# Performance work log

Measured on AMD Instinct MI355X. Metric: run time of the kernel, lower is better.

The kernel has to match this reference:

```python
import jax, jax.numpy as jnp
import numpy as np

# ---- model dims (match init_kwargs) ----
IN_DIM, HID, OUT, BRANCH = 700, 512, 20, 4
VTH = 1.0
B, T = 256, 250


def _make_mask(rng):
    # DH-SNN dendritic mask: for each hidden neuron, a random permutation of the
    # (padded) inputs is split into BRANCH contiguous groups; branch j of neuron i
    # only sees its group.  pad = ((IN//BR)*BR + BR - IN) % BR == 0 for 700/4.
    mask = np.zeros((HID * BRANCH, IN_DIM), dtype=np.float32)
    per = IN_DIM // BRANCH
    for i in range(HID):
        seq = rng.permutation(IN_DIM)
        for j in range(BRANCH):
            mask[i * BRANCH + j, seq[j * per:(j + 1) * per]] = 1.0
    return jnp.asarray(mask)


def setup_inputs() -> dict:
    key = jax.random.key(0)
    ks = jax.random.split(key, 8)
    x = jax.random.normal(ks[0], (B, T, IN_DIM), dtype=jnp.float32)
    # nn.Linear(IN, HID*BRANCH) style init
    lim1 = 1.0 / np.sqrt(IN_DIM)
    w1 = jax.random.uniform(ks[1], (HID * BRANCH, IN_DIM), jnp.float32, -lim1, lim1)
    b1 = jax.random.uniform(ks[2], (HID * BRANCH,), jnp.float32, -lim1, lim1)
    # tau initializer 'uniform' in [low_m, high_m] = [0, 4]
    tau_m1 = jax.random.uniform(ks[3], (HID,), jnp.float32, 0.0, 4.0)
    tau_n1 = jax.random.uniform(ks[4], (HID, BRANCH), jnp.float32, 0.0, 4.0)
    lim2 = 1.0 / np.sqrt(HID)
    w2 = jax.random.uniform(ks[5], (OUT, HID), jnp.float32, -lim2, lim2)
    b2 = jax.random.uniform(ks[6], (OUT,), jnp.float32, -lim2, lim2)
    tau_m2 = jax.random.uniform(ks[7], (OUT,), jnp.float32, 0.0, 4.0)
    mask = _make_mask(np.random.default_rng(0))
    return {"x": x, "w1": w1, "b1": b1, "tau_m1": tau_m1, "tau_n1": tau_n1,
            "mask": mask, "w2": w2, "b2": b2, "tau_m2": tau_m2}


# surrogate-gradient spike (ActFun_adp with gaussian surrogate; fwd = heaviside)
GAMMA, LENS = 0.5, 0.5

@jax.custom_vjp
def spike_fn(v):
    return (v > 0).astype(v.dtype)

def _spike_fwd(v):
    return spike_fn(v), v

def _spike_bwd(v, g):
    sg = GAMMA * jnp.exp(-(v * v) / (2.0 * LENS * LENS)) / jnp.sqrt(2.0 * jnp.pi * LENS * LENS)
    return (g * sg,)

spike_fn.defvjp(_spike_fwd, _spike_bwd)


def reference(x, w1, b1, tau_m1, tau_n1, mask, w2, b2, tau_m2):
    Bb, Tt, _ = x.shape
    H, K = tau_n1.shape
    O = tau_m2.shape[0]
    eff_w = w1 * mask                                   # masked dendritic weights
    # precompute branch currents for all timesteps in one GEMM: (B,T,H*K)
    cur = jnp.einsum('bti,hi->bth', x, eff_w) + b1
    cur = cur.reshape(Bb, Tt, H, K)
    beta = jax.nn.sigmoid(tau_n1)                        # (H,K) dendritic decay
    alpha = jax.nn.sigmoid(tau_m1)                       # (H,)  soma decay
    alpha2 = jax.nn.sigmoid(tau_m2)                      # (O,)  readout decay

    def step(carry, c_t):
        d, mem1, spk, mem2 = carry
        d = beta * d + (1.0 - beta) * c_t                # dendritic membrane
        l = d.sum(-1)                                    # (B,H) summed branches (wotanh)
        mem1 = alpha * mem1 + (1.0 - alpha) * l - VTH * spk  # soft reset
        spk = spike_fn(mem1 - VTH)
        mem2 = alpha2 * mem2 + (1.0 - alpha2) * (spk @ w2.T + b2)  # leaky readout
        return (d, mem1, spk, mem2), mem2

    init = (jnp.zeros((Bb, H, K), x.dtype), jnp.zeros((Bb, H), x.dtype),
            jnp.zeros((Bb, H), x.dtype), jnp.zeros((Bb, O), x.dtype))
    _, outs = jax.lax.scan(step, init, jnp.swapaxes(cur, 0, 1))
    return jnp.swapaxes(outs, 0, 1)                      # (B,T,O)
```

## Files before the change

kernel.cpp:

```cpp
#include <hip/hip_runtime.h>
#include <hip/hip_bf16.h>
#include <hip/hip_fp16.h>

#define BATCH 256
#define TSTEPS 250
#define INDIM 700
#define KPAD 704
#define HID 512
#define HK 2048
#define NOUT 20
#define NCHUNK 66

typedef __attribute__((ext_vector_type(8))) _Float16 f16x8;
typedef __attribute__((ext_vector_type(4))) _Float16 f16x4;
typedef __attribute__((ext_vector_type(4))) float f32x4;

__device__ __forceinline__ float sigf(float x) { return 1.0f / (1.0f + expf(-x)); }

__device__ __forceinline__ void gload_lds16(const void* g, void* l) {
    __builtin_amdgcn_global_load_lds(
        (const __attribute__((address_space(1))) void*)g,
        (__attribute__((address_space(3))) void*)l, 16, 0, 0);
}

__global__ __launch_bounds__(192) void split_x(
    const float* __restrict__ x, _Float16* __restrict__ X0,
    _Float16* __restrict__ X1, int t0, int tc) {
    const int row = blockIdx.x;
    const int b = row / tc, tt = row - b * tc;
    const float* xr = x + (size_t)(b * TSTEPS + t0 + tt) * INDIM;
    const int k = threadIdx.x * 4;
    if (k >= KPAD) return;
    float4 v = {0.f, 0.f, 0.f, 0.f};
    if (k < INDIM) v = *(const float4*)(xr + k);
    f16x4 h, l;
    h[0] = (_Float16)v.x; l[0] = (_Float16)(v.x - (float)h[0]);
    h[1] = (_Float16)v.y; l[1] = (_Float16)(v.y - (float)h[1]);
    h[2] = (_Float16)v.z; l[2] = (_Float16)(v.z - (float)h[2]);
    h[3] = (_Float16)v.w; l[3] = (_Float16)(v.w - (float)h[3]);
    *(f16x4*)(X0 + (size_t)row * KPAD + k) = h;
    *(f16x4*)(X1 + (size_t)row * KPAD + k) = l;
}

__global__ __launch_bounds__(192) void split_w(
    const float* __restrict__ w1, const float* __restrict__ mask,
    _Float16* __restrict__ W0, _Float16* __restrict__ W1) {
    const int n = blockIdx.x;
    const int k = threadIdx.x * 4;
    if (k >= KPAD) return;
    float4 e = {0.f, 0.f, 0.f, 0.f};
    if (k < INDIM) {
        float4 wv = *(const float4*)(w1 + (size_t)n * INDIM + k);
        float4 mv = *(const float4*)(mask + (size_t)n * INDIM + k);
        e.x = wv.x * mv.x; e.y = wv.y * mv.y;
        e.z = wv.z * mv.z; e.w = wv.w * mv.w;
    }
    f16x4 h, l;
    h[0] = (_Float16)e.x; l[0] = (_Float16)(e.x - (float)h[0]);
    h[1] = (_Float16)e.y; l[1] = (_Float16)(e.y - (float)h[1]);
    h[2] = (_Float16)e.z; l[2] = (_Float16)(e.z - (float)h[2]);
    h[3] = (_Float16)e.w; l[3] = (_Float16)(e.w - (float)h[3]);
    *(f16x4*)(W0 + (size_t)n * KPAD + k) = h;
    *(f16x4*)(W1 + (size_t)n * KPAD + k) = l;
}

__global__ __launch_bounds__(512, 1) void gemm_f16(
    const _Float16* __restrict__ X0, const _Float16* __restrict__ X1,
    const _Float16* __restrict__ W0, const _Float16* __restrict__ W1,
    const float* __restrict__ b1, float* __restrict__ C) {
    extern __shared__ char smem[];
    const int tid = threadIdx.x;
    const int w = tid >> 6, lane = tid & 63;
    const int wm = w >> 2, wn = w & 3;
    const int lm = lane & 15, cfr = lane >> 4;

    const int nwg = gridDim.x;
    const int cpx = nwg >> 3;
    const int o = blockIdx.x;
    const int wg = (o & 7) * cpx + (o >> 3);
    const int n0 = (wg & 7) * 256;
    const int m0 = (wg >> 3) * 256;

    size_t grA[2], grB[2];
#pragma unroll
    for (int i = 0; i < 2; ++i) {
        int pr = i * 64 + (tid >> 3);
        int p = tid & 7;
        int l = p ^ (pr & 7);
        int rr = 2 * pr + (l >> 2);
        int c = l & 3;
        grA[i] = (size_t)(m0 + rr) * (KPAD * 2) + (size_t)c * 16;
        grB[i] = (size_t)(n0 + rr) * (KPAD * 2) + (size_t)c * 16;
    }

    int aoff[8], boff[4];
#pragma unroll
    for (int mf = 0; mf < 8; ++mf) {
        int row = wm * 128 + mf * 16 + lm;
        int pr = row >> 1, l = (row & 1) * 4 + cfr, p = l ^ (pr & 7);
        aoff[mf] = pr * 128 + p * 16;
    }
#pragma unroll
    for (int nf = 0; nf < 4; ++nf) {
        int row = wn * 64 + nf * 16 + lm;
        int pr = row >> 1, l = (row & 1) * 4 + cfr, p = l ^ (pr & 7);
        boff[nf] = pr * 128 + p * 16;
    }

    auto stageA = [&](int js) {
        int seg = (js >= 44) ? 2 : (js >= 22 ? 1 : 0);
        const char* base = (const char*)((seg < 2) ? X0 : X1);
        size_t ko = (size_t)(js - seg * 22) * 64;
        char* l0 = smem + (js & 3) * 32768 + w * 1024;
        gload_lds16(base + grA[0] + ko, l0);
        gload_lds16(base + grA[1] + ko, l0 + 8192);
    };
    auto stageB = [&](int js) {
        int seg = (js >= 44) ? 2 : (js >= 22 ? 1 : 0);
        const char* base = (const char*)((seg == 1) ? W1 : W0);
        size_t ko = (size_t)(js - seg * 22) * 64;
        char* l0 = smem + (js & 3) * 32768 + 16384 + w * 1024;
        gload_lds16(base + grB[0] + ko, l0);
        gload_lds16(base + grB[1] + ko, l0 + 8192);
    };

    f32x4 acc[8][4];
#pragma unroll
    for (int mf = 0; mf < 8; ++mf)
#pragma unroll
        for (int nf = 0; nf < 4; ++nf) acc[mf][nf] = (f32x4){0.f, 0.f, 0.f, 0.f};

    stageA(0); stageB(0); stageA(1); stageB(1);
    asm volatile("s_waitcnt vmcnt(4)" ::: "memory");
    __builtin_amdgcn_s_barrier();
    __builtin_amdgcn_sched_barrier(0);

    for (int j = 0; j < NCHUNK; ++j) {
        const char* sa = smem + (j & 3) * 32768;
        const char* sb = sa + 16384;
        f16x8 alo[4], bf[4];
#pragma unroll
        for (int mf = 0; mf < 4; ++mf)
            alo[mf] = *(const f16x8*)(sa + aoff[mf]);
#pragma unroll
        for (int nf = 0; nf < 4; ++nf)
            bf[nf] = *(const f16x8*)(sb + boff[nf]);
        if (j + 2 < NCHUNK) stageA(j + 2);
        __builtin_amdgcn_s_barrier();
        __builtin_amdgcn_sched_barrier(0);
        __builtin_amdgcn_s_setprio(1);
#pragma unroll
        for (int mf = 0; mf < 4; ++mf)
#pragma unroll
            for (int nf = 0; nf < 4; ++nf)
                acc[mf][nf] = __builtin_amdgcn_mfma_f32_16x16x32_f16(
                    alo[mf], bf[nf], acc[mf][nf], 0, 0, 0);
        __builtin_amdgcn_s_setprio(0);
        __builtin_amdgcn_s_barrier();
        __builtin_amdgcn_sched_barrier(0);
        f16x8 ahi[4];
#pragma unroll
        for (int mf = 0; mf < 4; ++mf)
            ahi[mf] = *(const f16x8*)(sa + aoff[4 + mf]);
        if (j + 2 < NCHUNK) stageB(j + 2);
        if (j < NCHUNK - 2)
            asm volatile("s_waitcnt vmcnt(4)" ::: "memory");
        else
            asm volatile("s_waitcnt vmcnt(0)" ::: "memory");
        __builtin_amdgcn_s_barrier();
        __builtin_amdgcn_sched_barrier(0);
        __builtin_amdgcn_s_setprio(1);
#pragma unroll
        for (int mf = 0; mf < 4; ++mf)
#pragma unroll
            for (int nf = 0; nf < 4; ++nf)
                acc[4 + mf][nf] = __builtin_amdgcn_mfma_f32_16x16x32_f16(
                    ahi[mf], bf[nf], acc[4 + mf][nf], 0, 0, 0);
        __builtin_amdgcn_s_setprio(0);
        __builtin_amdgcn_s_barrier();
        __builtin_amdgcn_sched_barrier(0);
    }

    const int crow0 = m0 + wm * 128 + (lane >> 4) * 4;
    const int ccol0 = n0 + wn * 64 + lm;
#pragma unroll
    for (int nf = 0; nf < 4; ++nf) {
        const float bias = b1[ccol0 + nf * 16];
#pragma unroll
        for (int mf = 0; mf < 8; ++mf) {
            f32x4 v = acc[mf][nf];
            const int r0 = crow0 + mf * 16;
#pragma unroll
            for (int r = 0; r < 4; ++r)
                C[(size_t)(r0 + r) * HK + ccol0 + nf * 16] = v[r] + bias;
        }
    }
}

__global__ __launch_bounds__(256) void snn_scan(
    const float* __restrict__ Cur,
    const float* __restrict__ tau_m1,
    const float* __restrict__ tau_n1,
    float* __restrict__ st_d,
    float* __restrict__ st_m1,
    unsigned long long* __restrict__ spk,
    int t0, int tc) {
    const int b = blockIdx.x;
    const int tid = threadIdx.x;
    const int h0 = tid, h1 = tid + 256;
    const int wid = tid >> 6, lane = tid & 63;

    const float a0 = sigf(tau_m1[h0]);
    const float a1 = sigf(tau_m1[h1]);
    const float oma0 = 1.0f - a0, oma1 = 1.0f - a1;
    float4 tb0 = *(const float4*)(tau_n1 + h0 * 4);
    float4 tb1 = *(const float4*)(tau_n1 + h1 * 4);
    float be0[4] = {sigf(tb0.x), sigf(tb0.y), sigf(tb0.z), sigf(tb0.w)};
    float be1[4] = {sigf(tb1.x), sigf(tb1.y), sigf(tb1.z), sigf(tb1.w)};
    float ob0[4] = {1.0f - be0[0], 1.0f - be0[1], 1.0f - be0[2], 1.0f - be0[3]};
    float ob1[4] = {1.0f - be1[0], 1.0f - be1[1], 1.0f - be1[2], 1.0f - be1[3]};

    float d0[4], d1[4], m10, m11, s0, s1;
    if (t0 == 0) {
#pragma unroll
        for (int k = 0; k < 4; ++k) { d0[k] = 0.0f; d1[k] = 0.0f; }
        m10 = 0.0f; m11 = 0.0f; s0 = 0.0f; s1 = 0.0f;
    } else {
        float4 dv0 = *(const float4*)(st_d + (size_t)b * HK + tid * 4);
        float4 dv1 = *(const float4*)(st_d + (size_t)b * HK + 1024 + tid * 4);
        d0[0] = dv0.x; d0[1] = dv0.y; d0[2] = dv0.z; d0[3] = dv0.w;
        d1[0] = dv1.x; d1[1] = dv1.y; d1[2] = dv1.z; d1[3] = dv1.w;
        m10 = st_m1[(size_t)b * HID + h0];
        m11 = st_m1[(size_t)b * HID + h1];
        const unsigned long long* sp = spk + ((size_t)b * TSTEPS + (t0 - 1)) * 8;
        s0 = ((sp[wid] >> lane) & 1ull) ? 1.0f : 0.0f;
        s1 = ((sp[4 + wid] >> lane) & 1ull) ? 1.0f : 0.0f;
    }

    const float* cbase = Cur + (size_t)b * tc * HK;
    float4 c0 = *(const float4*)(cbase + tid * 4);
    float4 c1 = *(const float4*)(cbase + 1024 + tid * 4);

    for (int tt = 0; tt < tc; ++tt) {
        float4 n0v, n1v;
        if (tt + 1 < tc) {
            const float* p = cbase + (size_t)(tt + 1) * HK;
            n0v = *(const float4*)(p + tid * 4);
            n1v = *(const float4*)(p + 1024 + tid * 4);
        } else { n0v = c0; n1v = c1; }

        d0[0] = be0[0] * d0[0] + ob0[0] * c0.x;
        d0[1] = be0[1] * d0[1] + ob0[1] * c0.y;
        d0[2] = be0[2] * d0[2] + ob0[2] * c0.z;
        d0[3] = be0[3] * d0[3] + ob0[3] * c0.w;
        d1[0] = be1[0] * d1[0] + ob1[0] * c1.x;
        d1[1] = be1[1] * d1[1] + ob1[1] * c1.y;
        d1[2] = be1[2] * d1[2] + ob1[2] * c1.z;
        d1[3] = be1[3] * d1[3] + ob1[3] * c1.w;
        float l0 = (d0[0] + d0[1]) + (d0[2] + d0[3]);
        float l1 = (d1[0] + d1[1]) + (d1[2] + d1[3]);

        m10 = a0 * m10 + oma0 * l0 - s0;
        m11 = a1 * m11 + oma1 * l1 - s1;
        bool sp0 = m10 > 1.0f;
        bool sp1 = m11 > 1.0f;
        s0 = sp0 ? 1.0f : 0.0f;
        s1 = sp1 ? 1.0f : 0.0f;

        unsigned long long mk0 = __ballot(sp0);
        unsigned long long mk1 = __ballot(sp1);
        if (lane == 0) {
            unsigned long long* ox = spk + ((size_t)b * TSTEPS + (t0 + tt)) * 8;
            ox[wid] = mk0;
            ox[4 + wid] = mk1;
        }
        c0 = n0v; c1 = n1v;
    }

    float4 dv0 = {d0[0], d0[1], d0[2], d0[3]};
    float4 dv1 = {d1[0], d1[1], d1[2], d1[3]};
    *(float4*)(st_d + (size_t)b * HK + tid * 4) = dv0;
    *(float4*)(st_d + (size_t)b * HK + 1024 + tid * 4) = dv1;
    st_m1[(size_t)b * HID + h0] = m10;
    st_m1[(size_t)b * HID + h1] = m11;
}

__global__ __launch_bounds__(256) void spk_gemm(
    const unsigned long long* __restrict__ spk,
    const float* __restrict__ w2,
    const float* __restrict__ b2,
    float* __restrict__ Y) {
    __shared__ float w2t[512][21];
    const int t = blockIdx.x;
    const int b = threadIdx.x;
    for (int i = threadIdx.x; i < HID * NOUT; i += 256) {
        int o = i / HID;
        int h = i - o * HID;
        w2t[h][o] = w2[i];
    }
    __syncthreads();
    float acc[NOUT];
#pragma unroll
    for (int o = 0; o < NOUT; ++o) acc[o] = b2[o];
    const unsigned long long* sp = spk + ((size_t)b * TSTEPS + t) * 8;
#pragma unroll
    for (int w = 0; w < 8; ++w) {
        unsigned long long m = sp[w];
        while (m) {
            int i = __ffsll((long long)m) - 1;
            m &= m - 1;
            const float* col = &w2t[w * 64 + i][0];
#pragma unroll
            for (int o = 0; o < NOUT; ++o) acc[o] += col[o];
        }
    }
    float* outp = Y + ((size_t)b * TSTEPS + t) * NOUT;
#pragma unroll
    for (int o = 0; o < NOUT; ++o) outp[o] = acc[o];
}

__global__ __launch_bounds__(256) void filter_out(
    float* __restrict__ Y, const float* __restrict__ tau_m2) {
    int gid = blockIdx.x * 256 + threadIdx.x;
    if (gid >= BATCH * NOUT) return;
    int b = gid / NOUT;
    int o = gid - b * NOUT;
    float a2 = sigf(tau_m2[o]);
    float oma = 1.0f - a2;
    float m2 = 0.0f;
    float* p = Y + (size_t)b * TSTEPS * NOUT + o;
    for (int t = 0; t < TSTEPS; ++t) {
        m2 = a2 * m2 + oma * p[(size_t)t * NOUT];
        p[(size_t)t * NOUT] = m2;
    }
}

extern "C" void kernel_launch(void* const* d_in, const int* in_sizes, int n_in,
                              void* d_out, int out_size, void* d_ws, size_t ws_size,
                              hipStream_t stream) {
    const float* x      = (const float*)d_in[0];
    const float* w1     = (const float*)d_in[1];
    const float* b1     = (const float*)d_in[2];
    const float* tau_m1 = (const float*)d_in[3];
    const float* tau_n1 = (const float*)d_in[4];
    const float* mask   = (const float*)d_in[5];
    const float* w2     = (const float*)d_in[6];
    const float* b2     = (const float*)d_in[7];
    const float* tau_m2 = (const float*)d_in[8];
    float* out = (float*)d_out;

    char* ws = (char*)d_ws;
    size_t off = 0;
    auto walloc = [&](size_t bytes) -> void* {
        void* p = ws + off;
        off += (bytes + 255) & ~(size_t)255;
        return p;
    };
    _Float16* W0 = (_Float16*)walloc((size_t)HK * KPAD * 2);
    _Float16* W1 = (_Float16*)walloc((size_t)HK * KPAD * 2);
    unsigned long long* spk =
        (unsigned long long*)walloc((size_t)BATCH * TSTEPS * 8 * 8);
    float* st_d  = (float*)walloc((size_t)BATCH * HK * 4);
    float* st_m1 = (float*)walloc((size_t)BATCH * HID * 4);

    const size_t perT = (size_t)BATCH * HK * 4 + 2 * (size_t)BATCH * KPAD * 2;
    size_t avail = (ws_size > off + 4096) ? ws_size - off - 4096 : 0;
    int Tc = (int)(avail / perT);
    if (Tc > TSTEPS) Tc = TSTEPS;
    if (Tc < 1) Tc = 1;
    _Float16* X0 = (_Float16*)walloc((size_t)BATCH * Tc * KPAD * 2);
    _Float16* X1 = (_Float16*)walloc((size_t)BATCH * Tc * KPAD * 2);
    float* cur   = (float*)walloc((size_t)BATCH * Tc * HK * 4);

    split_w<<<HK, 192, 0, stream>>>(w1, mask, W0, W1);

    for (int t0 = 0; t0 < TSTEPS; t0 += Tc) {
        int tc = (TSTEPS - t0 < Tc) ? (TSTEPS - t0) : Tc;
        split_x<<<BATCH * tc, 192, 0, stream>>>(x, X0, X1, t0, tc);
        dim3 grid(8 * tc);
        gemm_f16<<<grid, 512, 131072, stream>>>(X0, X1, W0, W1, b1, cur);
        snn_scan<<<BATCH, 256, 0, stream>>>(cur, tau_m1, tau_n1, st_d, st_m1,
                                            spk, t0, tc);
    }
    spk_gemm<<<TSTEPS, 256, 0, stream>>>(spk, w2, b2, out);
    filter_out<<<(BATCH * NOUT + 255) / 256, 256, 0, stream>>>(out, tau_m2);
}
```

Before: 1.133 ms.

## Use 32x32 MFMA with deeper prefetch, split scan blocks, chunk readout filter

The GEMM moves from 16x16x32 to 32x32x16 MFMA tiles. It also stages three chunks ahead instead of two and drops half the barriers per iteration. The SNN scan now launches two blocks per batch row, each with one neuron per thread, to double parallelism. The serial readout leaky filter becomes a three-pass chunked scan (partial, combine, fix-up with powf decay) so more threads work on it. These changes raise MFMA efficiency and latency hiding, at the cost of more accumulator registers, extra kernel launches, and slight rounding differences in the filter.

After: 1.148 ms. About the same (+1.3%).

```diff
diff --git a/kernel.cpp b/kernel.cpp
--- a/kernel.cpp
+++ b/kernel.cpp
@@ -10,10 +10,13 @@
 #define HK 2048
 #define NOUT 20
 #define NCHUNK 66
+#define FCH 10
+#define FCL 25
 
 typedef __attribute__((ext_vector_type(8))) _Float16 f16x8;
 typedef __attribute__((ext_vector_type(4))) _Float16 f16x4;
 typedef __attribute__((ext_vector_type(4))) float f32x4;
+typedef __attribute__((ext_vector_type(16))) float f32x16;
 
 __device__ __forceinline__ float sigf(float x) { return 1.0f / (1.0f + expf(-x)); }
 
@@ -72,7 +75,7 @@
     const int tid = threadIdx.x;
     const int w = tid >> 6, lane = tid & 63;
     const int wm = w >> 2, wn = w & 3;
-    const int lm = lane & 15, cfr = lane >> 4;
+    const int lr = lane & 31, cl = lane >> 5;
 
     const int nwg = gridDim.x;
     const int cpx = nwg >> 3;
@@ -93,19 +96,25 @@
         grB[i] = (size_t)(n0 + rr) * (KPAD * 2) + (size_t)c * 16;
     }
 
-    int aoff[8], boff[4];
-#pragma unroll
-    for (int mf = 0; mf < 8; ++mf) {
-        int row = wm * 128 + mf * 16 + lm;
-        int pr = row >> 1, l = (row & 1) * 4 + cfr, p = l ^ (pr & 7);
-        aoff[mf] = pr * 128 + p * 16;
-    }
-#pragma unroll
-    for (int nf = 0; nf < 4; ++nf) {
-        int row = wn * 64 + nf * 16 + lm;
-        int pr = row >> 1, l = (row & 1) * 4 + cfr, p = l ^ (pr & 7);
-        boff[nf] = pr * 128 + p * 16;
-    }
+    int aoff[4][2], boff[2][2];
+#pragma unroll
+    for (int mb = 0; mb < 4; ++mb)
+#pragma unroll
+        for (int ks = 0; ks < 2; ++ks) {
+            int row = wm * 128 + mb * 32 + lr;
+            int c = ks * 2 + cl;
+            int pr = row >> 1, l = (row & 1) * 4 + c, p = l ^ (pr & 7);
+            aoff[mb][ks] = pr * 128 + p * 16;
+        }
+#pragma unroll
+    for (int nb = 0; nb < 2; ++nb)
+#pragma unroll
+        for (int ks = 0; ks < 2; ++ks) {
+            int row = wn * 64 + nb * 32 + lr;
+            int c = ks * 2 + cl;
+            int pr = row >> 1, l = (row & 1) * 4 + c, p = l ^ (pr & 7);
+            boff[nb][ks] = pr * 128 + p * 16;
+        }
 
     auto stageA = [&](int js) {
         int seg = (js >= 44) ? 2 : (js >= 22 ? 1 : 0);
@@ -124,75 +133,68 @@
         gload_lds16(base + grB[1] + ko, l0 + 8192);
     };
 
-    f32x4 acc[8][4];
-#pragma unroll
-    for (int mf = 0; mf < 8; ++mf)
-#pragma unroll
-        for (int nf = 0; nf < 4; ++nf) acc[mf][nf] = (f32x4){0.f, 0.f, 0.f, 0.f};
-
-    stageA(0); stageB(0); stageA(1); stageB(1);
-    asm volatile("s_waitcnt vmcnt(4)" ::: "memory");
+    f32x16 acc[4][2];
+#pragma unroll
+    for (int mb = 0; mb < 4; ++mb)
+#pragma unroll
+        for (int nb = 0; nb < 2; ++nb)
+#pragma unroll
+            for (int r = 0; r < 16; ++r) acc[mb][nb][r] = 0.f;
+
+    stageA(0); stageB(0); stageA(1); stageB(1); stageA(2); stageB(2);
+    asm volatile("s_waitcnt vmcnt(8)" ::: "memory");
     __builtin_amdgcn_s_barrier();
     __builtin_amdgcn_sched_barrier(0);
 
     for (int j = 0; j < NCHUNK; ++j) {
         const char* sa = smem + (j & 3) * 32768;
         const char* sb = sa + 16384;
-        f16x8 alo[4], bf[4];
-#pragma unroll
-        for (int mf = 0; mf < 4; ++mf)
-            alo[mf] = *(const f16x8*)(sa + aoff[mf]);
-#pragma unroll
-        for (int nf = 0; nf < 4; ++nf)
-            bf[nf] = *(const f16x8*)(sb + boff[nf]);
-        if (j + 2 < NCHUNK) stageA(j + 2);
-        __builtin_amdgcn_s_barrier();
-        __builtin_amdgcn_sched_barrier(0);
+        if (j + 3 < NCHUNK) { stageA(j + 3); stageB(j + 3); }
+        f16x8 af[4][2], bf[2][2];
+#pragma unroll
+        for (int mb = 0; mb < 4; ++mb)
+#pragma unroll
+            for (int ks = 0; ks < 2; ++ks)
+                af[mb][ks] = *(const f16x8*)(sa + aoff[mb][ks]);
+#pragma unroll
+        for (int nb = 0; nb < 2; ++nb)
+#pragma unroll
+            for (int ks = 0; ks < 2; ++ks)
+                bf[nb][ks] = *(const f16x8*)(sb + boff[nb][ks]);
         __builtin_amdgcn_s_setprio(1);
 #pragma unroll
-        for (int mf = 0; mf < 4; ++mf)
-#pragma unroll
-            for (int nf = 0; nf < 4; ++nf)
-                acc[mf][nf] = __builtin_amdgcn_mfma_f32_16x16x32_f16(
-                    alo[mf], bf[nf], acc[mf][nf], 0, 0, 0);
+        for (int ks = 0; ks < 2; ++ks)
+#pragma unroll
+            for (int mb = 0; mb < 4; ++mb)
+#pragma unroll
+                for (int nb = 0; nb < 2; ++nb)
+                    acc[mb][nb] = __builtin_amdgcn_mfma_f32_32x32x16_f16(
+                        af[mb][ks], bf[nb][ks], acc[mb][nb], 0, 0, 0);
         __builtin_amdgcn_s_setprio(0);
-        __builtin_amdgcn_s_barrier();
-        __builtin_amdgcn_sched_barrier(0);
-        f16x8 ahi[4];
-#pragma unroll
-        for (int mf = 0; mf < 4; ++mf)
-            ahi[mf] = *(const f16x8*)(sa + aoff[4 + mf]);
-        if (j + 2 < NCHUNK) stageB(j + 2);
-        if (j < NCHUNK - 2)
+        if (j < NCHUNK - 3)
+            asm volatile("s_waitcnt vmcnt(8)" ::: "memory");
+        else if (j == NCHUNK - 3)
             asm volatile("s_waitcnt vmcnt(4)" ::: "memory");
         else
             asm volatile("s_waitcnt vmcnt(0)" ::: "memory");
         __builtin_amdgcn_s_barrier();
         __builtin_amdgcn_sched_barrier(0);
-        __builtin_amdgcn_s_setprio(1);
-#pragma unroll
-        for (int mf = 0; mf < 4; ++mf)
-#pragma unroll
-            for (int nf = 0; nf < 4; ++nf)
-                acc[4 + mf][nf] = __builtin_amdgcn_mfma_f32_16x16x32_f16(
-                    ahi[mf], bf[nf], acc[4 + mf][nf], 0, 0, 0);
-        __builtin_amdgcn_s_setprio(0);
-        __builtin_amdgcn_s_barrier();
-        __builtin_amdgcn_sched_barrier(0);
-    }
-
-    const int crow0 = m0 + wm * 128 + (lane >> 4) * 4;
-    const int ccol0 = n0 + wn * 64 + lm;
-#pragma unroll
-    for (int nf = 0; nf < 4; ++nf) {
-        const float bias = b1[ccol0 + nf * 16];
-#pragma unroll
-        for (int mf = 0; mf < 8; ++mf) {
-            f32x4 v = acc[mf][nf];
-            const int r0 = crow0 + mf * 16;
-#pragma unroll
-            for (int r = 0; r < 4; ++r)
-                C[(size_t)(r0 + r) * HK + ccol0 + nf * 16] = v[r] + bias;
+    }
+
+    const int rbase = m0 + wm * 128 + 4 * cl;
+    const int col0 = n0 + wn * 64 + lr;
+#pragma unroll
+    for (int nb = 0; nb < 2; ++nb) {
+        const int col = col0 + nb * 32;
+        const float bias = b1[col];
+#pragma unroll
+        for (int mb = 0; mb < 4; ++mb) {
+            f32x16 v = acc[mb][nb];
+#pragma unroll
+            for (int r = 0; r < 16; ++r) {
+                int row = rbase + mb * 32 + (r & 3) + 8 * (r >> 2);
+                C[(size_t)row * HK + col] = v[r] + bias;
+            }
         }
     }
 }
@@ -206,83 +208,59 @@
     unsigned long long* __restrict__ spk,
     int t0, int tc) {
     const int b = blockIdx.x;
+    const int half = blockIdx.y;
     const int tid = threadIdx.x;
-    const int h0 = tid, h1 = tid + 256;
-    const int wid = tid >> 6, lane = tid & 63;
-
-    const float a0 = sigf(tau_m1[h0]);
-    const float a1 = sigf(tau_m1[h1]);
-    const float oma0 = 1.0f - a0, oma1 = 1.0f - a1;
-    float4 tb0 = *(const float4*)(tau_n1 + h0 * 4);
-    float4 tb1 = *(const float4*)(tau_n1 + h1 * 4);
-    float be0[4] = {sigf(tb0.x), sigf(tb0.y), sigf(tb0.z), sigf(tb0.w)};
-    float be1[4] = {sigf(tb1.x), sigf(tb1.y), sigf(tb1.z), sigf(tb1.w)};
-    float ob0[4] = {1.0f - be0[0], 1.0f - be0[1], 1.0f - be0[2], 1.0f - be0[3]};
-    float ob1[4] = {1.0f - be1[0], 1.0f - be1[1], 1.0f - be1[2], 1.0f - be1[3]};
-
-    float d0[4], d1[4], m10, m11, s0, s1;
+    const int h = half * 256 + tid;
+    const int wid = half * 4 + (tid >> 6), lane = tid & 63;
+    const int coff = half * 1024 + tid * 4;
+
+    const float a0 = sigf(tau_m1[h]);
+    const float oma0 = 1.0f - a0;
+    float4 tb = *(const float4*)(tau_n1 + h * 4);
+    float be[4] = {sigf(tb.x), sigf(tb.y), sigf(tb.z), sigf(tb.w)};
+    float ob[4] = {1.0f - be[0], 1.0f - be[1], 1.0f - be[2], 1.0f - be[3]};
+
+    float d[4], m1, s;
     if (t0 == 0) {
-#pragma unroll
-        for (int k = 0; k < 4; ++k) { d0[k] = 0.0f; d1[k] = 0.0f; }
-        m10 = 0.0f; m11 = 0.0f; s0 = 0.0f; s1 = 0.0f;
+        d[0] = d[1] = d[2] = d[3] = 0.0f;
+        m1 = 0.0f; s = 0.0f;
     } else {
-        float4 dv0 = *(const float4*)(st_d + (size_t)b * HK + tid * 4);
-        float4 dv1 = *(const float4*)(st_d + (size_t)b * HK + 1024 + tid * 4);
-        d0[0] = dv0.x; d0[1] = dv0.y; d0[2] = dv0.z; d0[3] = dv0.w;
-        d1[0] = dv1.x; d1[1] = dv1.y; d1[2] = dv1.z; d1[3] = dv1.w;
-        m10 = st_m1[(size_t)b * HID + h0];
-        m11 = st_m1[(size_t)b * HID + h1];
+        float4 dv = *(const float4*)(st_d + (size_t)b * HK + coff);
+        d[0] = dv.x; d[1] = dv.y; d[2] = dv.z; d[3] = dv.w;
+        m1 = st_m1[(size_t)b * HID + h];
         const unsigned long long* sp = spk + ((size_t)b * TSTEPS + (t0 - 1)) * 8;
-        s0 = ((sp[wid] >> lane) & 1ull) ? 1.0f : 0.0f;
-        s1 = ((sp[4 + wid] >> lane) & 1ull) ? 1.0f : 0.0f;
+        s = ((sp[wid] >> lane) & 1ull) ? 1.0f : 0.0f;
     }
 
     const float* cbase = Cur + (size_t)b * tc * HK;
-    float4 c0 = *(const float4*)(cbase + tid * 4);
-    float4 c1 = *(const float4*)(cbase + 1024 + tid * 4);
+    float4 c0 = *(const float4*)(cbase + coff);
 
     for (int tt = 0; tt < tc; ++tt) {
-        float4 n0v, n1v;
-        if (tt + 1 < tc) {
-            const float* p = cbase + (size_t)(tt + 1) * HK;
-            n0v = *(const float4*)(p + tid * 4);
-            n1v = *(const float4*)(p + 1024 + tid * 4);
-        } else { n0v = c0; n1v = c1; }
-
-        d0[0] = be0[0] * d0[0] + ob0[0] * c0.x;
-        d0[1] = be0[1] * d0[1] + ob0[1] * c0.y;
-        d0[2] = be0[2] * d0[2] + ob0[2] * c0.z;
-        d0[3] = be0[3] * d0[3] + ob0[3] * c0.w;
-        d1[0] = be1[0] * d1[0] + ob1[0] * c1.x;
-        d1[1] = be1[1] * d1[1] + ob1[1] * c1.y;
-        d1[2] = be1[2] * d1[2] + ob1[2] * c1.z;
-        d1[3] = be1[3] * d1[3] + ob1[3] * c1.w;
-        float l0 = (d0[0] + d0[1]) + (d0[2] + d0[3]);
-        float l1 = (d1[0] + d1[1]) + (d1[2] + d1[3]);
-
-        m10 = a0 * m10 + oma0 * l0 - s0;
-        m11 = a1 * m11 + oma1 * l1 - s1;
-        bool sp0 = m10 > 1.0f;
-        bool sp1 = m11 > 1.0f;
-        s0 = sp0 ? 1.0f : 0.0f;
-        s1 = sp1 ? 1.0f : 0.0f;
-
-        unsigned long long mk0 = __ballot(sp0);
-        unsigned long long mk1 = __ballot(sp1);
-        if (lane == 0) {
-            unsigned long long* ox = spk + ((size_t)b * TSTEPS + (t0 + tt)) * 8;
-            ox[wid] = mk0;
-            ox[4 + wid] = mk1;
-        }
-        c0 = n0v; c1 = n1v;
-    }
-
-    float4 dv0 = {d0[0], d0[1], d0[2], d0[3]};
-    float4 dv1 = {d1[0], d1[1], d1[2], d1[3]};
-    *(float4*)(st_d + (size_t)b * HK + tid * 4) = dv0;
-    *(float4*)(st_d + (size_t)b * HK + 1024 + tid * 4) = dv1;
-    st_m1[(size_t)b * HID + h0] = m10;
-    st_m1[(size_t)b * HID + h1] = m11;
+        float4 nv;
+        if (tt + 1 < tc)
+            nv = *(const float4*)(cbase + (size_t)(tt + 1) * HK + coff);
+        else
+            nv = c0;
+
+        d[0] = be[0] * d[0] + ob[0] * c0.x;
+        d[1] = be[1] * d[1] + ob[1] * c0.y;
+        d[2] = be[2] * d[2] + ob[2] * c0.z;
+        d[3] = be[3] * d[3] + ob[3] * c0.w;
+        float l = (d[0] + d[1]) + (d[2] + d[3]);
+
+        m1 = a0 * m1 + oma0 * l - s;
+        bool sp0 = m1 > 1.0f;
+        s = sp0 ? 1.0f : 0.0f;
+
+        unsigned long long mk = __ballot(sp0);
+        if (lane == 0)
+            spk[((size_t)b * TSTEPS + (t0 + tt)) * 8 + wid] = mk;
+        c0 = nv;
+    }
+
+    float4 dv = {d[0], d[1], d[2], d[3]};
+    *(float4*)(st_d + (size_t)b * HK + coff) = dv;
+    st_m1[(size_t)b * HID + h] = m1;
 }
 
 __global__ __launch_bounds__(256) void spk_gemm(
@@ -319,20 +297,53 @@
     for (int o = 0; o < NOUT; ++o) outp[o] = acc[o];
 }
 
-__global__ __launch_bounds__(256) void filter_out(
-    float* __restrict__ Y, const float* __restrict__ tau_m2) {
-    int gid = blockIdx.x * 256 + threadIdx.x;
-    if (gid >= BATCH * NOUT) return;
-    int b = gid / NOUT;
-    int o = gid - b * NOUT;
+__global__ __launch_bounds__(256) void filter_part(
+    float* __restrict__ Y, const float* __restrict__ tau_m2,
+    float* __restrict__ fin) {
+    int id = blockIdx.x * 256 + threadIdx.x;
+    if (id >= BATCH * NOUT * FCH) return;
+    int c = id / (BATCH * NOUT);
+    int rem = id - c * (BATCH * NOUT);
+    int b = rem / NOUT, o = rem - b * NOUT;
     float a2 = sigf(tau_m2[o]);
     float oma = 1.0f - a2;
-    float m2 = 0.0f;
-    float* p = Y + (size_t)b * TSTEPS * NOUT + o;
-    for (int t = 0; t < TSTEPS; ++t) {
-        m2 = a2 * m2 + oma * p[(size_t)t * NOUT];
-        p[(size_t)t * NOUT] = m2;
-    }
+    float m = 0.0f;
+    float* p = Y + ((size_t)b * TSTEPS + c * FCL) * NOUT + o;
+    for (int tt = 0; tt < FCL; ++tt) {
+        m = a2 * m + oma * p[(size_t)tt * NOUT];
+        p[(size_t)tt * NOUT] = m;
+    }
+    fin[id] = m;
+}
+
+__global__ __launch_bounds__(256) void filter_comb(
+    const float* __restrict__ tau_m2, float* __restrict__ fin) {
+    int id = blockIdx.x * 256 + threadIdx.x;
+    if (id >= BATCH * NOUT) return;
+    int o = id % NOUT;
+    float a2 = sigf(tau_m2[o]);
+    float aL = powf(a2, (float)FCL);
+    float m = 0.0f;
+    for (int c = 0; c < FCH; ++c) {
+        float f = fin[(size_t)c * (BATCH * NOUT) + id];
+        fin[(size_t)c * (BATCH * NOUT) + id] = m;
+        m = aL * m + f;
+    }
+}
+
+__global__ __launch_bounds__(256) void filter_fix(
+    float* __restrict__ Y, const float* __restrict__ tau_m2,
+    const float* __restrict__ fin) {
+    int id = blockIdx.x * 256 + threadIdx.x;
+    if (id >= BATCH * TSTEPS * NOUT) return;
+    int o = id % NOUT;
+    int bt = id / NOUT;
+    int t = bt % TSTEPS, b = bt / TSTEPS;
+    int c = t / FCL, tt = t - c * FCL;
+    float a2 = sigf(tau_m2[o]);
+    float m0 = fin[(size_t)c * (BATCH * NOUT) + b * NOUT + o];
+    if (m0 != 0.0f)
+        Y[id] += powf(a2, (float)(tt + 1)) * m0;
 }
 
 extern "C" void kernel_launch(void* const* d_in, const int* in_sizes, int n_in,
@@ -362,6 +373,7 @@
         (unsigned long long*)walloc((size_t)BATCH * TSTEPS * 8 * 8);
     float* st_d  = (float*)walloc((size_t)BATCH * HK * 4);
     float* st_m1 = (float*)walloc((size_t)BATCH * HID * 4);
+    float* fin   = (float*)walloc((size_t)BATCH * NOUT * FCH * 4);
 
     const size_t perT = (size_t)BATCH * HK * 4 + 2 * (size_t)BATCH * KPAD * 2;
     size_t avail = (ws_size > off + 4096) ? ws_size - off - 4096 : 0;
@@ -379,9 +391,12 @@
         split_x<<<BATCH * tc, 192, 0, stream>>>(x, X0, X1, t0, tc);
         dim3 grid(8 * tc);
         gemm_f16<<<grid, 512, 131072, stream>>>(X0, X1, W0, W1, b1, cur);
-        snn_scan<<<BATCH, 256, 0, stream>>>(cur, tau_m1, tau_n1, st_d, st_m1,
+        dim3 sgrid(BATCH, 2);
+        snn_scan<<<sgrid, 256, 0, stream>>>(cur, tau_m1, tau_n1, st_d, st_m1,
                                             spk, t0, tc);
     }
     spk_gemm<<<TSTEPS, 256, 0, stream>>>(spk, w2, b2, out);
-    filter_out<<<(BATCH * NOUT + 255) / 256, 256, 0, stream>>>(out, tau_m2);
-}
+    filter_part<<<(BATCH * NOUT * FCH + 255) / 256, 256, 0, stream>>>(out, tau_m2, fin);
+    filter_comb<<<(BATCH * NOUT + 255) / 256, 256, 0, stream>>>(tau_m2, fin);
+    filter_fix<<<(BATCH * TSTEPS * NOUT + 255) / 256, 256, 0, stream>>>(out, tau_m2, fin);
+}
```
